# Performance work log

Measured on AMD Instinct MI355X. Metric: run time of the kernel, lower is better.

Reference implementation:

```python
import jax, jax.numpy as jnp
import numpy as np

B, F, T, EPT, S, E, H, LVL = 16384, 512, 4, 2, 2, 256, 128, 2

def _ple_level(xs_task, x_sh, w_task, b_task, w_sh, b_sh, w_gate, b_gate, w_gsh=None, b_gsh=None):
    # xs_task: [T,B,I] per-task inputs; x_sh: [B,I] shared input
    task_out = jax.nn.relu(jnp.einsum('tbi,teio->tbeo', xs_task, w_task) + b_task[:, None])  # [T,B,EPT,E]
    sh_out = jax.nn.relu(jnp.einsum('bi,sio->bso', x_sh, w_sh) + b_sh)                       # [B,S,E]
    t = task_out.shape[0]
    experts = jnp.concatenate([task_out, jnp.broadcast_to(sh_out[None], (t,) + sh_out.shape)], axis=2)  # [T,B,EPT+S,E]
    gate = jax.nn.softmax(jnp.einsum('tbi,tig->tbg', xs_task, w_gate) + b_gate[:, None], axis=-1)
    task_next = jnp.einsum('tbg,tbge->tbe', gate, experts)  # [T,B,E]
    sh_next = None
    if w_gsh is not None:
        # all experts ordered task0_exp0, task0_exp1, task1_exp0, ..., then shared
        bsz = x_sh.shape[0]
        all_exp = jnp.concatenate([jnp.transpose(task_out, (1, 0, 2, 3)).reshape(bsz, -1, task_out.shape[-1]), sh_out], axis=1)
        gsh = jax.nn.softmax(x_sh @ w_gsh + b_gsh, axis=-1)
        sh_next = jnp.einsum('bg,bge->be', gsh, all_exp)
    return task_next, sh_next

def setup_inputs() -> dict:
    key = jax.random.key(0)
    ks = jax.random.split(key, 16)
    sc = 0.02
    d = {
        'x': jax.random.normal(ks[0], (B, F), jnp.float32),
        # level 0 (in_dim=F, has shared gate)
        'w_task0': jax.random.normal(ks[1], (T, EPT, F, E), jnp.float32) * sc,
        'b_task0': jnp.zeros((T, EPT, E), jnp.float32),
        'w_sh0': jax.random.normal(ks[2], (S, F, E), jnp.float32) * sc,
        'b_sh0': jnp.zeros((S, E), jnp.float32),
        'w_gate0': jax.random.normal(ks[3], (T, F, EPT + S), jnp.float32) * sc,
        'b_gate0': jnp.zeros((T, EPT + S), jnp.float32),
        'w_gsh0': jax.random.normal(ks[4], (F, T * EPT + S), jnp.float32) * sc,
        'b_gsh0': jnp.zeros((T * EPT + S,), jnp.float32),
        # level 1 (last; in_dim=E, no shared gate)
        'w_task1': jax.random.normal(ks[5], (T, EPT, E, E), jnp.float32) * sc,
        'b_task1': jnp.zeros((T, EPT, E), jnp.float32),
        'w_sh1': jax.random.normal(ks[6], (S, E, E), jnp.float32) * sc,
        'b_sh1': jnp.zeros((S, E), jnp.float32),
        'w_gate1': jax.random.normal(ks[7], (T, E, EPT + S), jnp.float32) * sc,
        'b_gate1': jnp.zeros((T, EPT + S), jnp.float32),
        # towers
        'w_tw': jax.random.normal(ks[8], (T, E, H), jnp.float32) * sc,
        'b_tw': jnp.zeros((T, H), jnp.float32),
        'w_out': jax.random.normal(ks[9], (T, H, 2), jnp.float32) * sc,
        'b_out': jnp.zeros((T, 2), jnp.float32),
    }
    return d

def reference(x, w_task0, b_task0, w_sh0, b_sh0, w_gate0, b_gate0, w_gsh0, b_gsh0,
              w_task1, b_task1, w_sh1, b_sh1, w_gate1, b_gate1,
              w_tw, b_tw, w_out, b_out):
    xs_task = jnp.broadcast_to(x[None], (T,) + x.shape)  # all tasks see same input at level 0
    t1, sh1 = _ple_level(xs_task, x, w_task0, b_task0, w_sh0, b_sh0, w_gate0, b_gate0, w_gsh0, b_gsh0)
    t2, _ = _ple_level(t1, sh1, w_task1, b_task1, w_sh1, b_sh1, w_gate1, b_gate1)
    h = jax.nn.relu(jnp.einsum('tbe,teh->tbh', t2, w_tw) + b_tw[:, None])
    logits = jnp.einsum('tbh,tho->tbo', h, w_out) + b_out[:, None]
    p = jax.nn.softmax(logits, axis=-1)
    return jnp.clip(p, 1e-15, 1.0 - 1e-15)  # [T,B,2]
```

## Files before the change

### kernel.cpp

```cpp
#include <hip/hip_runtime.h>

typedef unsigned short u16;
typedef __bf16 bf16x8 __attribute__((ext_vector_type(8)));
typedef float f32x4 __attribute__((ext_vector_type(4)));
typedef u16 u16x8 __attribute__((ext_vector_type(8)));

#define B_ 16384

__device__ __forceinline__ u16 f2b(float f){
  unsigned u = __builtin_bit_cast(unsigned, f);
  u = (u + 0x7FFFu + ((u >> 16) & 1u)) >> 16;
  return (u16)u;
}
__device__ __forceinline__ float b2f(u16 v){
  return __builtin_bit_cast(float, ((unsigned)v) << 16);
}
__device__ __forceinline__ void ld8(const u16* __restrict__ p, float* f){
  u16x8 v = *(const u16x8*)p;
  #pragma unroll
  for (int j = 0; j < 8; ++j) f[j] = b2f(v[j]);
}
__device__ __forceinline__ void st8(u16* __restrict__ p, const float* f){
  u16x8 v;
  #pragma unroll
  for (int j = 0; j < 8; ++j) v[j] = f2b(f[j]);
  *(u16x8*)p = v;
}

__device__ __forceinline__ void gload16(const u16* g, u16* lds){
  __builtin_amdgcn_global_load_lds(
      (const __attribute__((address_space(1))) unsigned int*)g,
      (__attribute__((address_space(3))) unsigned int*)lds, 16, 0, 0);
}

__device__ __forceinline__ void core256_8p(const u16* __restrict__ A,
                                           const u16* __restrict__ Wt,
                                           int K, int m0, int n0, int nt,
                                           u16* sm, f32x4 acc[8][4])
{
  const int tid = threadIdx.x, lane = tid & 63;
  const int wm = (tid >> 8) * 128;
  const int wn = ((tid >> 6) & 3) * 64;

  #pragma unroll
  for (int m = 0; m < 8; ++m)
    #pragma unroll
    for (int n = 0; n < 4; ++n) acc[m][n] = (f32x4){0.f, 0.f, 0.f, 0.f};

  const int srow  = tid >> 3;
  const int sslot = (tid & 7) ^ (srow & 7);
  const u16* psrc[8];
  int pdst[8];
  const int wbase = (tid >> 6) * 512;
  #pragma unroll
  for (int g = 0; g < 4; ++g) {
    psrc[g]     = A  + (size_t)(m0 + g * 64 + srow) * K + sslot * 8;
    pdst[g]     = g * 4096 + wbase;
    psrc[g + 4] = Wt + (size_t)(n0 + g * 64 + srow) * K + sslot * 8;
    pdst[g + 4] = 16384 + g * 4096 + wbase;
  }

  int abase[2], bbase[2];
  #pragma unroll
  for (int kk = 0; kk < 2; ++kk) {
    int phys = (kk * 4 + (lane >> 4)) ^ (lane & 7);
    abase[kk] = (wm + (lane & 15)) * 64 + phys * 8;
    bbase[kk] = 16384 + (wn + (lane & 15)) * 64 + phys * 8;
  }

  gload16(psrc[4], sm + pdst[4]); gload16(psrc[5], sm + pdst[5]);
  gload16(psrc[6], sm + pdst[6]); gload16(psrc[7], sm + pdst[7]);
  gload16(psrc[0], sm + pdst[0]); gload16(psrc[2], sm + pdst[2]);
  gload16(psrc[1], sm + pdst[1]); gload16(psrc[3], sm + pdst[3]);
  asm volatile("s_waitcnt vmcnt(2)" ::: "memory");
  __builtin_amdgcn_s_barrier();

  for (int t = 0; t < nt; ++t) {
    const u16* s = sm + (t & 1) * 32768;
    u16* d = sm + ((t + 1) & 1) * 32768;
    const bool nx = (t + 1 < nt);
    const size_t ko = (size_t)(t + 1) * 64;
    bf16x8 bv0[4], bv1[4], av[4];

    #pragma unroll
    for (int n = 0; n < 4; ++n) bv0[n] = *(const bf16x8*)(s + bbase[0] + n * 1024);
    #pragma unroll
    for (int m = 0; m < 4; ++m) av[m] = *(const bf16x8*)(s + abase[0] + m * 1024);
    if (nx) { gload16(psrc[4] + ko, d + pdst[4]); gload16(psrc[5] + ko, d + pdst[5]); }
    __builtin_amdgcn_s_barrier();
    asm volatile("s_waitcnt lgkmcnt(0)" ::: "memory");
    __builtin_amdgcn_s_setprio(1);
    #pragma unroll
    for (int m = 0; m < 4; ++m)
      #pragma unroll
      for (int n = 0; n < 4; ++n)
        acc[m][n] = __builtin_amdgcn_mfma_f32_16x16x32_bf16(av[m], bv0[n], acc[m][n], 0, 0, 0);
    __builtin_amdgcn_s_setprio(0);
    __builtin_amdgcn_s_barrier();

    #pragma unroll
    for (int n = 0; n < 4; ++n) bv1[n] = *(const bf16x8*)(s + bbase[1] + n * 1024);
    #pragma unroll
    for (int m = 0; m < 4; ++m) av[m] = *(const bf16x8*)(s + abase[1] + m * 1024);
    if (nx) { gload16(psrc[6] + ko, d + pdst[6]); gload16(psrc[7] + ko, d + pdst[7]); }
    __builtin_amdgcn_s_barrier();
    asm volatile("s_waitcnt lgkmcnt(0)" ::: "memory");
    __builtin_amdgcn_s_setprio(1);
    #pragma unroll
    for (int m = 0; m < 4; ++m)
      #pragma unroll
      for (int n = 0; n < 4; ++n)
        acc[m][n] = __builtin_amdgcn_mfma_f32_16x16x32_bf16(av[m], bv1[n], acc[m][n], 0, 0, 0);
    __builtin_amdgcn_s_setprio(0);
    if (nx) asm volatile("s_waitcnt vmcnt(4)" ::: "memory");
    else    asm volatile("s_waitcnt vmcnt(0)" ::: "memory");
    __builtin_amdgcn_s_barrier();

    #pragma unroll
    for (int m = 0; m < 4; ++m) av[m] = *(const bf16x8*)(s + abase[0] + (4 + m) * 1024);
    if (nx) { gload16(psrc[0] + ko, d + pdst[0]); gload16(psrc[2] + ko, d + pdst[2]); }
    __builtin_amdgcn_s_barrier();
    asm volatile("s_waitcnt lgkmcnt(0)" ::: "memory");
    __builtin_amdgcn_s_setprio(1);
    #pragma unroll
    for (int m = 0; m < 4; ++m)
      #pragma unroll
      for (int n = 0; n < 4; ++n)
        acc[4 + m][n] = __builtin_amdgcn_mfma_f32_16x16x32_bf16(av[m], bv0[n], acc[4 + m][n], 0, 0, 0);
    __builtin_amdgcn_s_setprio(0);
    __builtin_amdgcn_s_barrier();

    #pragma unroll
    for (int m = 0; m < 4; ++m) av[m] = *(const bf16x8*)(s + abase[1] + (4 + m) * 1024);
    if (nx) { gload16(psrc[1] + ko, d + pdst[1]); gload16(psrc[3] + ko, d + pdst[3]); }
    __builtin_amdgcn_s_barrier();
    asm volatile("s_waitcnt lgkmcnt(0)" ::: "memory");
    __builtin_amdgcn_s_setprio(1);
    #pragma unroll
    for (int m = 0; m < 4; ++m)
      #pragma unroll
      for (int n = 0; n < 4; ++n)
        acc[4 + m][n] = __builtin_amdgcn_mfma_f32_16x16x32_bf16(av[m], bv1[n], acc[4 + m][n], 0, 0, 0);
    __builtin_amdgcn_s_setprio(0);
    if (nx) asm volatile("s_waitcnt vmcnt(2)" ::: "memory");
    __builtin_amdgcn_s_barrier();
  }
}


__global__ __launch_bounds__(512) void k_gemm0(const u16* __restrict__ xb,
    const u16* __restrict__ Wt0, const float* __restrict__ bias0,
    u16* __restrict__ E0, float* __restrict__ G0L)
{
  __shared__ __align__(16) u16 sm[65536];
  f32x4 acc[8][4];
  const int bid = blockIdx.x;
  const int swz = (bid & 7) * 88 + (bid >> 3);
  const int m0 = (swz / 11) * 256, n0 = (swz % 11) * 256;
  core256_8p(xb, Wt0, 512, m0, n0, 8, sm, acc);
  const int lane = threadIdx.x & 63;
  const int wm = (threadIdx.x >> 8) * 128, wn = ((threadIdx.x >> 6) & 3) * 64;
  #pragma unroll
  for (int mi = 0; mi < 8; ++mi)
    #pragma unroll
    for (int ni = 0; ni < 4; ++ni) {
      int gcol = n0 + wn + ni * 16 + (lane & 15);
      float bias = bias0[gcol];
      #pragma unroll
      for (int q = 0; q < 4; ++q) {
        int grow = m0 + wm + mi * 16 + ((lane >> 4) << 2) + q;
        float v = acc[mi][ni][q] + bias;
        if (gcol < 2560)      E0[(size_t)grow * 2560 + gcol] = f2b(fmaxf(v, 0.f));
        else if (gcol < 2586) G0L[(size_t)grow * 26 + (gcol - 2560)] = v;
      }
    }
}

__global__ __launch_bounds__(256) void k_mix0(const u16* __restrict__ E0,
    const float* __restrict__ G0L, const float* __restrict__ WG1T,
    const float* __restrict__ b_gate1, u16* __restrict__ T1SH,
    float* __restrict__ G1S)
{
  const int b = blockIdx.x * 8 + (threadIdx.x >> 5);
  const int e0 = (threadIdx.x & 31) * 8;
  const float* gl = G0L + (size_t)b * 26;
  float g[4][4];
  #pragma unroll
  for (int t = 0; t < 4; ++t) {
    float l0 = gl[t*4+0], l1 = gl[t*4+1], l2 = gl[t*4+2], l3 = gl[t*4+3];
    float m = fmaxf(fmaxf(l0, l1), fmaxf(l2, l3));
    float e0e = expf(l0-m), e1 = expf(l1-m), e2 = expf(l2-m), e3 = expf(l3-m);
    float inv = 1.f / (e0e + e1 + e2 + e3);
    g[t][0] = e0e*inv; g[t][1] = e1*inv; g[t][2] = e2*inv; g[t][3] = e3*inv;
  }
  float gs[10];
  {
    float m = gl[16];
    #pragma unroll
    for (int j = 1; j < 10; ++j) m = fmaxf(m, gl[16 + j]);
    float s = 0.f;
    #pragma unroll
    for (int j = 0; j < 10; ++j) { gs[j] = expf(gl[16 + j] - m); s += gs[j]; }
    float inv = 1.f / s;
    #pragma unroll
    for (int j = 0; j < 10; ++j) gs[j] *= inv;
  }
  const u16* row = E0 + (size_t)b * 2560;
  float sh0[8], sh1[8], shacc[8];
  ld8(row + 2048 + e0, sh0);
  ld8(row + 2304 + e0, sh1);
  #pragma unroll
  for (int j = 0; j < 8; ++j) shacc[j] = gs[8]*sh0[j] + gs[9]*sh1[j];
  float gp[16];
  #pragma unroll
  for (int t = 0; t < 4; ++t) {
    float te0[8], te1[8], v[8];
    ld8(row + (t*2+0)*256 + e0, te0);
    ld8(row + (t*2+1)*256 + e0, te1);
    #pragma unroll
    for (int j = 0; j < 8; ++j) {
      v[j] = g[t][0]*te0[j] + g[t][1]*te1[j] + g[t][2]*sh0[j] + g[t][3]*sh1[j];
      shacc[j] += gs[t*2+0]*te0[j] + gs[t*2+1]*te1[j];
    }
    st8(T1SH + ((size_t)t * B_ + b) * 256 + e0, v);
    #pragma unroll
    for (int gg = 0; gg < 4; ++gg) {
      const float* wv = WG1T + ((size_t)(t * 4 + gg) * 256 + e0);
      float s = 0.f;
      #pragma unroll
      for (int j = 0; j < 8; ++j) s += v[j] * wv[j];
      gp[t * 4 + gg] = s;
    }
  }
  st8(T1SH + ((size_t)4 * B_ + b) * 256 + e0, shacc);
  #pragma unroll
  for (int i = 0; i < 16; ++i) {
    #pragma unroll
    for (int off = 1; off < 32; off <<= 1)
      gp[i] += __shfl_xor(gp[i], off, 32);
  }
  if ((threadIdx.x & 31) == 0) {
    float* orow = G1S + (size_t)b * 16;
    #pragma unroll
    for (int z = 0; z < 4; ++z) {
      float l0 = gp[z*4+0] + b_gate1[z*4+0];
      float l1 = gp[z*4+1] + b_gate1[z*4+1];
      float l2 = gp[z*4+2] + b_gate1[z*4+2];
      float l3 = gp[z*4+3] + b_gate1[z*4+3];
      float m = fmaxf(fmaxf(l0, l1), fmaxf(l2, l3));
      float x0 = expf(l0-m), x1 = expf(l1-m), x2 = expf(l2-m), x3 = expf(l3-m);
      float inv = 1.f / (x0 + x1 + x2 + x3);
      orow[z*4+0] = x0*inv; orow[z*4+1] = x1*inv;
      orow[z*4+2] = x2*inv; orow[z*4+3] = x3*inv;
    }
  }
}

__global__ __launch_bounds__(512) void k_gemm1(const u16* __restrict__ T1SH,
    const u16* __restrict__ Wt1, const float* __restrict__ bias1,
    u16* __restrict__ E1, u16* __restrict__ SH1E)
{
  __shared__ __align__(16) u16 sm[65536];
  f32x4 acc[8][4];
  const int bid = blockIdx.x;
  const int swz = (bid & 7) * 80 + (bid >> 3);
  const int mi_ = swz / 10, pan = swz % 10;
  const int z  = (pan < 8) ? (pan >> 1) : 4;
  const int n0 = (pan < 8) ? (pan & 1) * 256 : (pan - 8) * 256;
  const int m0 = mi_ * 256;
  core256_8p(T1SH + (size_t)z * B_ * 256, Wt1 + (size_t)z * 512 * 256, 256, m0, n0, 4, sm, acc);
  const int lane = threadIdx.x & 63;
  const int wm = (threadIdx.x >> 8) * 128, wn = ((threadIdx.x >> 6) & 3) * 64;
  const float* bias = bias1 + z * 512;
  #pragma unroll
  for (int mi = 0; mi < 8; ++mi)
    #pragma unroll
    for (int ni = 0; ni < 4; ++ni) {
      int gcol = n0 + wn + ni * 16 + (lane & 15);
      float bv = bias[gcol];
      #pragma unroll
      for (int q = 0; q < 4; ++q) {
        int grow = m0 + wm + mi * 16 + ((lane >> 4) << 2) + q;
        float v = fmaxf(acc[mi][ni][q] + bv, 0.f);
        if (z < 4) E1[((size_t)z * B_ + grow) * 512 + gcol] = f2b(v);
        else       SH1E[(size_t)grow * 512 + gcol] = f2b(v);
      }
    }
}

__global__ __launch_bounds__(256) void k_mix1(const u16* __restrict__ E1,
    const float* __restrict__ G1S, const u16* __restrict__ SH1E, u16* __restrict__ T2)
{
  const int b = blockIdx.x * 8 + (threadIdx.x >> 5);
  const int e0 = (threadIdx.x & 31) * 8;
  float sh0[8], sh1[8];
  ld8(SH1E + (size_t)b * 512 + e0, sh0);
  ld8(SH1E + (size_t)b * 512 + 256 + e0, sh1);
  const float* gr = G1S + (size_t)b * 16;
  #pragma unroll
  for (int t = 0; t < 4; ++t) {
    float g0 = gr[t*4+0], g1 = gr[t*4+1], g2 = gr[t*4+2], g3 = gr[t*4+3];
    float te0[8], te1[8], v[8];
    ld8(E1 + ((size_t)t * B_ + b) * 512 + e0, te0);
    ld8(E1 + ((size_t)t * B_ + b) * 512 + 256 + e0, te1);
    #pragma unroll
    for (int j = 0; j < 8; ++j)
      v[j] = g0*te0[j] + g1*te1[j] + g2*sh0[j] + g3*sh1[j];
    st8(T2 + ((size_t)t * B_ + b) * 256 + e0, v);
  }
}

__device__ __forceinline__ void gemm_core4(const u16* __restrict__ A,
                                           const u16* __restrict__ Wt,
                                           int K, int m0, int n0, int nt,
                                           u16* sm, f32x4 acc[4][4])
{
  const int tid  = threadIdx.x;
  const int lane = tid & 63;
  const int wave = tid >> 6;
  const int wm   = ((tid >> 7) & 1) * 64;
  const int wn   = ((tid >> 6) & 1) * 64;

  f32x4 zero = {0.f, 0.f, 0.f, 0.f};
  #pragma unroll
  for (int mi = 0; mi < 4; ++mi)
    #pragma unroll
    for (int ni = 0; ni < 4; ++ni) acc[mi][ni] = zero;

  const int srow  = lane >> 3;
  const int gslot = (lane & 7) ^ srow;
  const u16* gsrc[8];
  int gdst[8];
  #pragma unroll
  for (int i = 0; i < 8; ++i) {
    int c = wave * 8 + i;
    if (c < 16) {
      gsrc[i] = A + (size_t)(m0 + c * 8 + srow) * K + gslot * 8;
      gdst[i] = c * 512;
    } else {
      gsrc[i] = Wt + (size_t)(n0 + (c - 16) * 8 + srow) * K + gslot * 8;
      gdst[i] = 8192 + (c - 16) * 512;
    }
  }

  int aoff[2][4], boff[2][4];
  #pragma unroll
  for (int kk = 0; kk < 2; ++kk) {
    #pragma unroll
    for (int m = 0; m < 4; ++m) {
      int r = wm + m * 16 + (lane & 15);
      aoff[kk][m] = r * 64 + (((kk * 4 + (lane >> 4)) ^ (r & 7)) * 8);
    }
    #pragma unroll
    for (int n = 0; n < 4; ++n) {
      int r = wn + n * 16 + (lane & 15);
      boff[kk][n] = 8192 + r * 64 + (((kk * 4 + (lane >> 4)) ^ (r & 7)) * 8);
    }
  }

  #pragma unroll
  for (int i = 0; i < 8; ++i) gload16(gsrc[i], sm + gdst[i]);
  asm volatile("s_waitcnt vmcnt(0)" ::: "memory");
  __builtin_amdgcn_s_barrier();

  for (int j = 0; j < nt; ++j) {
    if (j + 1 < nt) {
      u16* base = sm + ((j + 1) & 1) * 16384;
      #pragma unroll
      for (int i = 0; i < 8; ++i) gload16(gsrc[i] + (size_t)(j + 1) * 64, base + gdst[i]);
    }
    const u16* sa = sm + (j & 1) * 16384;
    #pragma unroll
    for (int kk = 0; kk < 2; ++kk) {
      bf16x8 av[4], bv[4];
      #pragma unroll
      for (int m = 0; m < 4; ++m) av[m] = *(const bf16x8*)(sa + aoff[kk][m]);
      #pragma unroll
      for (int n = 0; n < 4; ++n) bv[n] = *(const bf16x8*)(sa + boff[kk][n]);
      #pragma unroll
      for (int m = 0; m < 4; ++m)
        #pragma unroll
        for (int n = 0; n < 4; ++n)
          acc[m][n] = __builtin_amdgcn_mfma_f32_16x16x32_bf16(av[m], bv[n], acc[m][n], 0, 0, 0);
    }
    if (j + 1 < nt) {
      asm volatile("s_waitcnt vmcnt(0)" ::: "memory");
      __builtin_amdgcn_s_barrier();
    }
  }
}

__global__ __launch_bounds__(256) void k_tower(const u16* __restrict__ T2,
    const u16* __restrict__ Wtw, const float* __restrict__ b_tw,
    const float* __restrict__ w_out, const float* __restrict__ b_out,
    float* __restrict__ out)
{
  __shared__ __align__(16) u16 sm[32768];
  __shared__ float part[2][128][2];
  f32x4 acc[4][4];
  const int z = blockIdx.z;
  const int m0 = blockIdx.x * 128;
  gemm_core4(T2 + (size_t)z * B_ * 256, Wtw + (size_t)z * 128 * 256, 256, m0, 0, 4, sm, acc);
  const int lane = threadIdx.x & 63;
  const int wm = ((threadIdx.x >> 7) & 1) * 64, wn = ((threadIdx.x >> 6) & 1) * 64;
  #pragma unroll
  for (int mi = 0; mi < 4; ++mi) {
    #pragma unroll
    for (int r = 0; r < 4; ++r) {
      float p0 = 0.f, p1 = 0.f;
      #pragma unroll
      for (int ni = 0; ni < 4; ++ni) {
        int col = wn + ni * 16 + (lane & 15);
        float h = fmaxf(acc[mi][ni][r] + b_tw[z * 128 + col], 0.f);
        p0 += h * w_out[(z * 128 + col) * 2 + 0];
        p1 += h * w_out[(z * 128 + col) * 2 + 1];
      }
      #pragma unroll
      for (int off = 1; off < 16; off <<= 1) {
        p0 += __shfl_xor(p0, off);
        p1 += __shfl_xor(p1, off);
      }
      if ((lane & 15) == 0) {
        int rowl = wm + mi * 16 + ((lane >> 4) << 2) + r;
        part[wn >> 6][rowl][0] = p0;
        part[wn >> 6][rowl][1] = p1;
      }
    }
  }
  __syncthreads();
  if (threadIdx.x < 128) {
    int rowl = threadIdx.x;
    float l0 = part[0][rowl][0] + part[1][rowl][0] + b_out[z * 2 + 0];
    float l1 = part[0][rowl][1] + part[1][rowl][1] + b_out[z * 2 + 1];
    float mx = fmaxf(l0, l1);
    float e0 = expf(l0 - mx), e1 = expf(l1 - mx);
    float inv = 1.f / (e0 + e1);
    float p0 = fminf(fmaxf(e0 * inv, 1e-15f), 1.0f);
    float p1 = fminf(fmaxf(e1 * inv, 1e-15f), 1.0f);
    size_t o = ((size_t)z * B_ + m0 + rowl) * 2;
    out[o] = p0; out[o + 1] = p1;
  }
}

__global__ void k_prep(const float* __restrict__ x,
    const float* __restrict__ w_task0, const float* __restrict__ b_task0,
    const float* __restrict__ w_sh0,   const float* __restrict__ b_sh0,
    const float* __restrict__ w_gate0, const float* __restrict__ b_gate0,
    const float* __restrict__ w_gsh0,  const float* __restrict__ b_gsh0,
    const float* __restrict__ w_task1, const float* __restrict__ b_task1,
    const float* __restrict__ w_sh1,   const float* __restrict__ b_sh1,
    const float* __restrict__ w_gate1, const float* __restrict__ w_tw,
    u16* __restrict__ xb, u16* __restrict__ Wt0, float* __restrict__ bias0,
    u16* __restrict__ Wt1, float* __restrict__ bias1, u16* __restrict__ Wtw,
    float* __restrict__ WG1T)
{
  size_t i = (size_t)blockIdx.x * 256 + threadIdx.x;
  const size_t S_X8  = (size_t)16384 * 512 / 8;
  const size_t S_WT0 = (size_t)2816 * 512;
  const size_t S_B0  = 2816;
  const size_t S_WT1 = (size_t)5 * 512 * 256;
  const size_t S_B1  = 5 * 512;
  const size_t S_WTW = (size_t)4 * 128 * 256;
  const size_t S_WG1 = 4096;

  if (i < S_X8) {
    size_t o = i * 8;
    float4 a = *(const float4*)(x + o);
    float4 b = *(const float4*)(x + o + 4);
    u16x8 v;
    v[0] = f2b(a.x); v[1] = f2b(a.y); v[2] = f2b(a.z); v[3] = f2b(a.w);
    v[4] = f2b(b.x); v[5] = f2b(b.y); v[6] = f2b(b.z); v[7] = f2b(b.w);
    *(u16x8*)(xb + o) = v;
    return;
  }
  i -= S_X8;
  if (i < S_WT0) {
    int c = (int)(i / 512), f = (int)(i % 512);
    float v = 0.f;
    if (c < 2048)      { int te = c >> 8, o = c & 255; v = w_task0[((size_t)te * 512 + f) * 256 + o]; }
    else if (c < 2560) { int s = (c - 2048) >> 8, o = c & 255; v = w_sh0[((size_t)s * 512 + f) * 256 + o]; }
    else if (c < 2576) { int q = c - 2560; int t = q >> 2, gg = q & 3; v = w_gate0[((size_t)t * 512 + f) * 4 + gg]; }
    else if (c < 2586) { int j = c - 2576; v = w_gsh0[(size_t)f * 10 + j]; }
    Wt0[i] = f2b(v);
    return;
  }
  i -= S_WT0;
  if (i < S_B0) {
    int c = (int)i; float v = 0.f;
    if (c < 2048)      { int te = c >> 8, o = c & 255; v = b_task0[te * 256 + o]; }
    else if (c < 2560) { int s = (c - 2048) >> 8, o = c & 255; v = b_sh0[s * 256 + o]; }
    else if (c < 2576) { v = b_gate0[c - 2560]; }
    else if (c < 2586) { v = b_gsh0[c - 2576]; }
    bias0[c] = v;
    return;
  }
  i -= S_B0;
  if (i < S_WT1) {
    int z = (int)(i / (512 * 256)); int rem = (int)(i % (512 * 256));
    int c = rem / 256, f = rem % 256;
    float v;
    if (z < 4) { int ee = c >> 8, o = c & 255; v = w_task1[(((size_t)(z * 2 + ee)) * 256 + f) * 256 + o]; }
    else       { int s = c >> 8, o = c & 255; v = w_sh1[((size_t)s * 256 + f) * 256 + o]; }
    Wt1[i] = f2b(v);
    return;
  }
  i -= S_WT1;
  if (i < S_B1) {
    int z = (int)(i / 512); int c = (int)(i % 512);
    float v;
    if (z < 4) { int ee = c >> 8, o = c & 255; v = b_task1[(z * 2 + ee) * 256 + o]; }
    else       { int s = c >> 8, o = c & 255; v = b_sh1[s * 256 + o]; }
    bias1[(size_t)z * 512 + c] = v;
    return;
  }
  i -= S_B1;
  if (i < S_WTW) {
    int z = (int)(i / (128 * 256)); int rem = (int)(i % (128 * 256));
    int h = rem / 256, f = rem % 256;
    Wtw[i] = f2b(w_tw[((size_t)z * 256 + f) * 128 + h]);
    return;
  }
  i -= S_WTW;
  if (i < S_WG1) {
    int t = (int)(i >> 10), gg = (int)((i >> 8) & 3), e = (int)(i & 255);
    WG1T[i] = w_gate1[((size_t)t * 256 + e) * 4 + gg];
    return;
  }
}

extern "C" void kernel_launch(void* const* d_in, const int* in_sizes, int n_in,
                              void* d_out, int out_size, void* d_ws, size_t ws_size,
                              hipStream_t stream)
{
  (void)in_sizes; (void)n_in; (void)out_size; (void)ws_size;
  const float* x       = (const float*)d_in[0];
  const float* w_task0 = (const float*)d_in[1];
  const float* b_task0 = (const float*)d_in[2];
  const float* w_sh0   = (const float*)d_in[3];
  const float* b_sh0   = (const float*)d_in[4];
  const float* w_gate0 = (const float*)d_in[5];
  const float* b_gate0 = (const float*)d_in[6];
  const float* w_gsh0  = (const float*)d_in[7];
  const float* b_gsh0  = (const float*)d_in[8];
  const float* w_task1 = (const float*)d_in[9];
  const float* b_task1 = (const float*)d_in[10];
  const float* w_sh1   = (const float*)d_in[11];
  const float* b_sh1   = (const float*)d_in[12];
  const float* w_gate1 = (const float*)d_in[13];
  const float* b_gate1 = (const float*)d_in[14];
  const float* w_tw    = (const float*)d_in[15];
  const float* b_tw    = (const float*)d_in[16];
  const float* w_out   = (const float*)d_in[17];
  const float* b_out   = (const float*)d_in[18];
  float* out = (float*)d_out;

  char* ws = (char*)d_ws;
  u16*   XB    = (u16*)  (ws + 0);
  u16*   SH1E  = (u16*)  (ws + 0);
  u16*   WT0   = (u16*)  (ws + 16777216);
  float* BIAS0 = (float*)(ws + 19660800);
  u16*   WT1   = (u16*)  (ws + 19672064);
  float* BIAS1 = (float*)(ws + 20982784);
  u16*   WTW   = (u16*)  (ws + 20993024);
  u16*   E0    = (u16*)  (ws + 21255168);
  u16*   T2    = (u16*)  (ws + 21255168);
  float* G0L   = (float*)(ws + 105141248);
  u16*   T1SH  = (u16*)  (ws + 106845184);
  u16*   E1    = (u16*)  (ws + 148788224);
  float* G1S   = (float*)(ws + 215897088);
  float* WG1T  = (float*)(ws + 216945664);

  k_prep<<<12837, 256, 0, stream>>>(x, w_task0, b_task0, w_sh0, b_sh0, w_gate0, b_gate0,
      w_gsh0, b_gsh0, w_task1, b_task1, w_sh1, b_sh1, w_gate1, w_tw,
      XB, WT0, BIAS0, WT1, BIAS1, WTW, WG1T);
  k_gemm0<<<704, 512, 0, stream>>>(XB, WT0, BIAS0, E0, G0L);
  k_mix0<<<2048, 256, 0, stream>>>(E0, G0L, WG1T, b_gate1, T1SH, G1S);
  k_gemm1<<<640, 512, 0, stream>>>(T1SH, WT1, BIAS1, E1, SH1E);
  k_mix1<<<2048, 256, 0, stream>>>(E1, G1S, SH1E, T2);
  k_tower<<<dim3(128, 1, 4), 256, 0, stream>>>(T2, WTW, b_tw, w_out, b_out, out);
}
```

Baseline: 193.6 us.

## Replace 256x256 GEMM core with 256x128 tile, K=32 triple-buffered pipeline

Swaps the 256x256 tile, K=64 double-buffered GEMM core for a 256x128 tile with K-steps of 32 and a three-stage LDS ring that prefetches two steps ahead. Each step now needs one barrier instead of four. Shared memory per block drops from 128KB to 72KB, and both GEMM grids double in block count. The aim is more blocks resident per CU, fewer wasted padded columns in gemm0 (2586 columns padded to 21x128 instead of 11x256), and less barrier overhead. In exchange each K step does half the MFMAs per LDS load and reuse of A per block falls.

Measured after the change: 179.1 us. -7.5%, faster.

```diff
diff --git a/kernel.cpp b/kernel.cpp
--- a/kernel.cpp
+++ b/kernel.cpp
@@ -33,117 +33,87 @@
       (__attribute__((address_space(3))) unsigned int*)lds, 16, 0, 0);
 }
 
-__device__ __forceinline__ void core256_8p(const u16* __restrict__ A,
-                                           const u16* __restrict__ Wt,
-                                           int K, int m0, int n0, int nt,
-                                           u16* sm, f32x4 acc[8][4])
-{
-  const int tid = threadIdx.x, lane = tid & 63;
-  const int wm = (tid >> 8) * 128;
-  const int wn = ((tid >> 6) & 3) * 64;
-
-  #pragma unroll
-  for (int m = 0; m < 8; ++m)
+__device__ __forceinline__ void core32(const u16* __restrict__ A,
+                                       const u16* __restrict__ Wt,
+                                       int K, int m0, int n0, int nt,
+                                       u16* sm, f32x4 acc[4][4])
+{
+  const int tid = threadIdx.x, lane = tid & 63, wave = tid >> 6;
+  const int wm = ((tid >> 7) & 3) * 64;
+  const int wn = ((tid >> 6) & 1) * 64;
+
+  #pragma unroll
+  for (int m = 0; m < 4; ++m)
     #pragma unroll
     for (int n = 0; n < 4; ++n) acc[m][n] = (f32x4){0.f, 0.f, 0.f, 0.f};
 
-  const int srow  = tid >> 3;
-  const int sslot = (tid & 7) ^ (srow & 7);
-  const u16* psrc[8];
-  int pdst[8];
-  const int wbase = (tid >> 6) * 512;
-  #pragma unroll
-  for (int g = 0; g < 4; ++g) {
-    psrc[g]     = A  + (size_t)(m0 + g * 64 + srow) * K + sslot * 8;
-    pdst[g]     = g * 4096 + wbase;
-    psrc[g + 4] = Wt + (size_t)(n0 + g * 64 + srow) * K + sslot * 8;
-    pdst[g + 4] = 16384 + g * 4096 + wbase;
-  }
-
-  int abase[2], bbase[2];
-  #pragma unroll
-  for (int kk = 0; kk < 2; ++kk) {
-    int phys = (kk * 4 + (lane >> 4)) ^ (lane & 7);
-    abase[kk] = (wm + (lane & 15)) * 64 + phys * 8;
-    bbase[kk] = 16384 + (wn + (lane & 15)) * 64 + phys * 8;
-  }
-
-  gload16(psrc[4], sm + pdst[4]); gload16(psrc[5], sm + pdst[5]);
-  gload16(psrc[6], sm + pdst[6]); gload16(psrc[7], sm + pdst[7]);
-  gload16(psrc[0], sm + pdst[0]); gload16(psrc[2], sm + pdst[2]);
-  gload16(psrc[1], sm + pdst[1]); gload16(psrc[3], sm + pdst[3]);
-  asm volatile("s_waitcnt vmcnt(2)" ::: "memory");
+  const int s_    = (lane & 7) ^ ((lane >> 3) & 7);
+  const int srow2 = 2 * (lane >> 3) + (s_ >> 2);
+  const int sk    = (s_ & 3) * 8;
+  const u16* gsrc[3];
+  int gdst[3];
+  #pragma unroll
+  for (int i = 0; i < 3; ++i) {
+    int c = wave * 3 + i;
+    if (c < 16) {
+      gsrc[i] = A + (size_t)(m0 + c * 16 + srow2) * K + sk;
+      gdst[i] = c * 512;
+    } else {
+      gsrc[i] = Wt + (size_t)(n0 + (c - 16) * 16 + srow2) * K + sk;
+      gdst[i] = 8192 + (c - 16) * 512;
+    }
+  }
+
+  int aoff[4], boff[4];
+  #pragma unroll
+  for (int m = 0; m < 4; ++m) {
+    int r = wm + m * 16 + (lane & 15);
+    int L = r >> 1;
+    int phys = (((r & 1) << 2) + (lane >> 4)) ^ (L & 7);
+    aoff[m] = L * 64 + phys * 8;
+  }
+  #pragma unroll
+  for (int n = 0; n < 4; ++n) {
+    int r = wn + n * 16 + (lane & 15);
+    int L = r >> 1;
+    int phys = (((r & 1) << 2) + (lane >> 4)) ^ (L & 7);
+    boff[n] = 8192 + L * 64 + phys * 8;
+  }
+
+  #pragma unroll
+  for (int j = 0; j < 2; ++j) {
+    u16* sl = sm + j * 12288;
+    #pragma unroll
+    for (int i = 0; i < 3; ++i) gload16(gsrc[i] + j * 32, sl + gdst[i]);
+  }
+  asm volatile("s_waitcnt vmcnt(3)" ::: "memory");
   __builtin_amdgcn_s_barrier();
 
-  for (int t = 0; t < nt; ++t) {
-    const u16* s = sm + (t & 1) * 32768;
-    u16* d = sm + ((t + 1) & 1) * 32768;
-    const bool nx = (t + 1 < nt);
-    const size_t ko = (size_t)(t + 1) * 64;
-    bf16x8 bv0[4], bv1[4], av[4];
-
-    #pragma unroll
-    for (int n = 0; n < 4; ++n) bv0[n] = *(const bf16x8*)(s + bbase[0] + n * 1024);
-    #pragma unroll
-    for (int m = 0; m < 4; ++m) av[m] = *(const bf16x8*)(s + abase[0] + m * 1024);
-    if (nx) { gload16(psrc[4] + ko, d + pdst[4]); gload16(psrc[5] + ko, d + pdst[5]); }
+  int cs = 0;
+  for (int j = 0; j < nt; ++j) {
+    if (j + 2 < nt) {
+      int ns = cs + 2; ns = (ns >= 3) ? ns - 3 : ns;
+      u16* sl = sm + ns * 12288;
+      #pragma unroll
+      for (int i = 0; i < 3; ++i) gload16(gsrc[i] + (size_t)(j + 2) * 32, sl + gdst[i]);
+    }
+    const u16* sa = sm + cs * 12288;
+    bf16x8 av[4], bv[4];
+    #pragma unroll
+    for (int m = 0; m < 4; ++m) av[m] = *(const bf16x8*)(sa + aoff[m]);
+    #pragma unroll
+    for (int n = 0; n < 4; ++n) bv[n] = *(const bf16x8*)(sa + boff[n]);
+    __builtin_amdgcn_s_setprio(1);
+    #pragma unroll
+    for (int m = 0; m < 4; ++m)
+      #pragma unroll
+      for (int n = 0; n < 4; ++n)
+        acc[m][n] = __builtin_amdgcn_mfma_f32_16x16x32_bf16(av[m], bv[n], acc[m][n], 0, 0, 0);
+    __builtin_amdgcn_s_setprio(0);
+    if (j + 2 < nt)      asm volatile("s_waitcnt vmcnt(3)" ::: "memory");
+    else if (j + 1 < nt) asm volatile("s_waitcnt vmcnt(0)" ::: "memory");
     __builtin_amdgcn_s_barrier();
-    asm volatile("s_waitcnt lgkmcnt(0)" ::: "memory");
-    __builtin_amdgcn_s_setprio(1);
-    #pragma unroll
-    for (int m = 0; m < 4; ++m)
-      #pragma unroll
-      for (int n = 0; n < 4; ++n)
-        acc[m][n] = __builtin_amdgcn_mfma_f32_16x16x32_bf16(av[m], bv0[n], acc[m][n], 0, 0, 0);
-    __builtin_amdgcn_s_setprio(0);
-    __builtin_amdgcn_s_barrier();
-
-    #pragma unroll
-    for (int n = 0; n < 4; ++n) bv1[n] = *(const bf16x8*)(s + bbase[1] + n * 1024);
-    #pragma unroll
-    for (int m = 0; m < 4; ++m) av[m] = *(const bf16x8*)(s + abase[1] + m * 1024);
-    if (nx) { gload16(psrc[6] + ko, d + pdst[6]); gload16(psrc[7] + ko, d + pdst[7]); }
-    __builtin_amdgcn_s_barrier();
-    asm volatile("s_waitcnt lgkmcnt(0)" ::: "memory");
-    __builtin_amdgcn_s_setprio(1);
-    #pragma unroll
-    for (int m = 0; m < 4; ++m)
-      #pragma unroll
-      for (int n = 0; n < 4; ++n)
-        acc[m][n] = __builtin_amdgcn_mfma_f32_16x16x32_bf16(av[m], bv1[n], acc[m][n], 0, 0, 0);
-    __builtin_amdgcn_s_setprio(0);
-    if (nx) asm volatile("s_waitcnt vmcnt(4)" ::: "memory");
-    else    asm volatile("s_waitcnt vmcnt(0)" ::: "memory");
-    __builtin_amdgcn_s_barrier();
-
-    #pragma unroll
-    for (int m = 0; m < 4; ++m) av[m] = *(const bf16x8*)(s + abase[0] + (4 + m) * 1024);
-    if (nx) { gload16(psrc[0] + ko, d + pdst[0]); gload16(psrc[2] + ko, d + pdst[2]); }
-    __builtin_amdgcn_s_barrier();
-    asm volatile("s_waitcnt lgkmcnt(0)" ::: "memory");
-    __builtin_amdgcn_s_setprio(1);
-    #pragma unroll
-    for (int m = 0; m < 4; ++m)
-      #pragma unroll
-      for (int n = 0; n < 4; ++n)
-        acc[4 + m][n] = __builtin_amdgcn_mfma_f32_16x16x32_bf16(av[m], bv0[n], acc[4 + m][n], 0, 0, 0);
-    __builtin_amdgcn_s_setprio(0);
-    __builtin_amdgcn_s_barrier();
-
-    #pragma unroll
-    for (int m = 0; m < 4; ++m) av[m] = *(const bf16x8*)(s + abase[1] + (4 + m) * 1024);
-    if (nx) { gload16(psrc[1] + ko, d + pdst[1]); gload16(psrc[3] + ko, d + pdst[3]); }
-    __builtin_amdgcn_s_barrier();
-    asm volatile("s_waitcnt lgkmcnt(0)" ::: "memory");
-    __builtin_amdgcn_s_setprio(1);
-    #pragma unroll
-    for (int m = 0; m < 4; ++m)
-      #pragma unroll
-      for (int n = 0; n < 4; ++n)
-        acc[4 + m][n] = __builtin_amdgcn_mfma_f32_16x16x32_bf16(av[m], bv1[n], acc[4 + m][n], 0, 0, 0);
-    __builtin_amdgcn_s_setprio(0);
-    if (nx) asm volatile("s_waitcnt vmcnt(2)" ::: "memory");
-    __builtin_amdgcn_s_barrier();
+    cs = (cs == 2) ? 0 : cs + 1;
   }
 }
 
@@ -152,16 +122,16 @@
     const u16* __restrict__ Wt0, const float* __restrict__ bias0,
     u16* __restrict__ E0, float* __restrict__ G0L)
 {
-  __shared__ __align__(16) u16 sm[65536];
-  f32x4 acc[8][4];
+  __shared__ __align__(16) u16 sm[36864];
+  f32x4 acc[4][4];
   const int bid = blockIdx.x;
-  const int swz = (bid & 7) * 88 + (bid >> 3);
-  const int m0 = (swz / 11) * 256, n0 = (swz % 11) * 256;
-  core256_8p(xb, Wt0, 512, m0, n0, 8, sm, acc);
+  const int swz = (bid & 7) * 168 + (bid >> 3);
+  const int m0 = (swz / 21) * 256, n0 = (swz % 21) * 128;
+  core32(xb, Wt0, 512, m0, n0, 16, sm, acc);
   const int lane = threadIdx.x & 63;
-  const int wm = (threadIdx.x >> 8) * 128, wn = ((threadIdx.x >> 6) & 3) * 64;
-  #pragma unroll
-  for (int mi = 0; mi < 8; ++mi)
+  const int wm = ((threadIdx.x >> 7) & 3) * 64, wn = ((threadIdx.x >> 6) & 1) * 64;
+  #pragma unroll
+  for (int mi = 0; mi < 4; ++mi)
     #pragma unroll
     for (int ni = 0; ni < 4; ++ni) {
       int gcol = n0 + wn + ni * 16 + (lane & 15);
@@ -260,20 +230,20 @@
     const u16* __restrict__ Wt1, const float* __restrict__ bias1,
     u16* __restrict__ E1, u16* __restrict__ SH1E)
 {
-  __shared__ __align__(16) u16 sm[65536];
-  f32x4 acc[8][4];
+  __shared__ __align__(16) u16 sm[36864];
+  f32x4 acc[4][4];
   const int bid = blockIdx.x;
-  const int swz = (bid & 7) * 80 + (bid >> 3);
-  const int mi_ = swz / 10, pan = swz % 10;
-  const int z  = (pan < 8) ? (pan >> 1) : 4;
-  const int n0 = (pan < 8) ? (pan & 1) * 256 : (pan - 8) * 256;
+  const int swz = (bid & 7) * 160 + (bid >> 3);
+  const int mi_ = swz / 20, pan = swz % 20;
+  const int z  = pan >> 2;
+  const int n0 = (pan & 3) * 128;
   const int m0 = mi_ * 256;
-  core256_8p(T1SH + (size_t)z * B_ * 256, Wt1 + (size_t)z * 512 * 256, 256, m0, n0, 4, sm, acc);
+  core32(T1SH + (size_t)z * B_ * 256, Wt1 + (size_t)z * 512 * 256, 256, m0, n0, 8, sm, acc);
   const int lane = threadIdx.x & 63;
-  const int wm = (threadIdx.x >> 8) * 128, wn = ((threadIdx.x >> 6) & 3) * 64;
+  const int wm = ((threadIdx.x >> 7) & 3) * 64, wn = ((threadIdx.x >> 6) & 1) * 64;
   const float* bias = bias1 + z * 512;
   #pragma unroll
-  for (int mi = 0; mi < 8; ++mi)
+  for (int mi = 0; mi < 4; ++mi)
     #pragma unroll
     for (int ni = 0; ni < 4; ++ni) {
       int gcol = n0 + wn + ni * 16 + (lane & 15);
@@ -573,9 +543,9 @@
   k_prep<<<12837, 256, 0, stream>>>(x, w_task0, b_task0, w_sh0, b_sh0, w_gate0, b_gate0,
       w_gsh0, b_gsh0, w_task1, b_task1, w_sh1, b_sh1, w_gate1, w_tw,
       XB, WT0, BIAS0, WT1, BIAS1, WTW, WG1T);
-  k_gemm0<<<704, 512, 0, stream>>>(XB, WT0, BIAS0, E0, G0L);
+  k_gemm0<<<1344, 512, 0, stream>>>(XB, WT0, BIAS0, E0, G0L);
   k_mix0<<<2048, 256, 0, stream>>>(E0, G0L, WG1T, b_gate1, T1SH, G1S);
-  k_gemm1<<<640, 512, 0, stream>>>(T1SH, WT1, BIAS1, E1, SH1E);
+  k_gemm1<<<1280, 512, 0, stream>>>(T1SH, WT1, BIAS1, E1, SH1E);
   k_mix1<<<2048, 256, 0, stream>>>(E1, G1S, SH1E, T2);
   k_tower<<<dim3(128, 1, 4), 256, 0, stream>>>(T2, WTW, b_tw, w_out, b_out, out);
 }
```
